# Performance work log

Hardware: AMD Instinct MI355X
Metric: run time of the kernel (lower is better)

## Reference

```python
import jax, jax.numpy as jnp
import numpy as np

EPS_NORM = 1e-12  # torch F.normalize eps
EPS_POOL = 1e-06
GAMMA = 10.0
TOPK = 32


def _l2norm(x, axis):
    n = jnp.sqrt(jnp.sum(x * x, axis=axis, keepdims=True))
    return x / jnp.maximum(n, EPS_NORM)


def _sae(x, enc, dec_w, dec_b):
    # x: [N, D]; enc: [H, D]; dec_w: [D, H]; dec_b: [D]
    w = _l2norm(enc, axis=1)
    x_n = _l2norm(x, axis=-1)
    cos = jnp.clip(x_n @ w.T, -1.0, 1.0)           # [N, H]
    acts = 2.0 - jnp.sqrt(2.0 - 2.0 * cos)
    vals, idx = jax.lax.top_k(acts, TOPK)           # [N, K]
    rows = jnp.arange(acts.shape[0])[:, None]
    sparse = jnp.zeros_like(acts).at[rows, idx].set(vals)
    recon = sparse @ dec_w.T + dec_b                # [N, D]
    return recon, sparse


def _sample_views(v_pad, centers, H, W):
    # v_pad: [B, Lmax, D], centers: [B, K, 2]; uniform grid HxW per batch
    L = H * W
    y = (jnp.arange(H, dtype=jnp.float32) + 0.5) / H
    x = (jnp.arange(W, dtype=jnp.float32) + 0.5) / W
    gy, gx = jnp.meshgrid(y, x, indexing='ij')
    coords = jnp.stack([gx.ravel(), gy.ravel()], axis=-1)        # [L, 2] (x, y)
    diff = centers[:, :, None, :] - coords[None, None, :, :]     # [B, K, L, 2]
    m = jnp.exp(-GAMMA * jnp.sum(diff * diff, axis=-1))          # [B, K, L]
    num = jnp.einsum('bkl,bld->bkd', m, v_pad[:, :L, :])
    den = jnp.sum(m, axis=-1, keepdims=True) + EPS_POOL
    return num / den                                             # [B, K, D]


def setup_inputs() -> dict:
    key = jax.random.key(0)
    ks = jax.random.split(key, 10)
    B, Lmax, D, Hh, T, K = 64, 1024, 1024, 16384, 512, 8
    fan_in = D
    bound = 1.0 / np.sqrt(fan_in)
    return {
        'v_pad': jax.random.normal(ks[0], (B, Lmax, D), jnp.float32),
        'v_len': jnp.full((B,), Lmax, dtype=jnp.int32),
        'grid_thws': jnp.tile(jnp.array([[1, 32, 32]], dtype=jnp.int32), (B, 1)),
        't_pad': jax.random.normal(ks[1], (B, T, D), jnp.float32),
        't_mask': jnp.ones((B, T), jnp.float32),
        'centers': jax.random.uniform(ks[2], (B, K, 2), jnp.float32),
        'enc_v': jax.random.normal(ks[3], (Hh, D), jnp.float32) * 0.02,
        'dec_v_w': jax.random.uniform(ks[4], (D, Hh), jnp.float32, -bound, bound),
        'dec_v_b': jnp.zeros((D,), jnp.float32),
        'enc_t': jax.random.normal(ks[5], (Hh, D), jnp.float32) * 0.02,
        'dec_t_w': jax.random.uniform(ks[6], (D, Hh), jnp.float32, -bound, bound),
        'dec_t_b': jnp.zeros((D,), jnp.float32),
    }


def reference(v_pad, v_len, grid_thws, t_pad, t_mask, centers,
              enc_v, dec_v_w, dec_v_b, enc_t, dec_t_w, dec_t_b):
    H = int(np.asarray(grid_thws)[0, 1])
    W = int(np.asarray(grid_thws)[0, 2])
    # text global pooling
    t_sum = jnp.sum(t_pad * t_mask[..., None], axis=1)
    t_global = t_sum / (jnp.sum(t_mask, axis=1, keepdims=True) + EPS_POOL)
    # gaussian view pooling
    v_views = _sample_views(v_pad, centers, H, W)                 # [B, K, D]
    recon_t, latent_t = _sae(t_global, enc_t, dec_t_w, dec_t_b)
    B, K, D = v_views.shape
    recon_v_flat, latent_v_flat = _sae(v_views.reshape(B * K, D), enc_v, dec_v_w, dec_v_b)
    recon_v = recon_v_flat.reshape(B, K, D)
    latent_v = latent_v_flat.reshape(B, K, -1)
    return (recon_v, v_views, recon_t, t_global, latent_v, latent_t)
```

## Files before the change

kernel.cpp:

```cpp
#include <hip/hip_runtime.h>
#include <hip/hip_bf16.h>

constexpr int NB    = 64;
constexpr int LMAX  = 1024;
constexpr int DD    = 1024;
constexpr int HSAE  = 16384;
constexpr int TT    = 512;
constexpr int KV    = 8;
constexpr int TOPK  = 32;
constexpr int NROW_V = NB * KV;
constexpr int NROW_T = NB;

constexpr size_t OUT_RECON_V = 0;
constexpr size_t OUT_VVIEWS  = OUT_RECON_V + (size_t)NROW_V * DD;
constexpr size_t OUT_RECON_T = OUT_VVIEWS + (size_t)NROW_V * DD;
constexpr size_t OUT_TGLOBAL = OUT_RECON_T + (size_t)NROW_T * DD;
constexpr size_t OUT_LAT_V   = OUT_TGLOBAL + (size_t)NROW_T * DD;
constexpr size_t OUT_LAT_T   = OUT_LAT_V + (size_t)NROW_V * HSAE;

constexpr size_t WS_VN     = 0;
constexpr size_t WS_TN     = WS_VN + (size_t)NROW_V * DD;
constexpr size_t WS_IDX_V  = WS_TN + (size_t)NROW_T * DD;
constexpr size_t WS_VAL_V  = WS_IDX_V + (size_t)NROW_V * TOPK;
constexpr size_t WS_IDX_T  = WS_VAL_V + (size_t)NROW_V * TOPK;
constexpr size_t WS_VAL_T  = WS_IDX_T + (size_t)NROW_T * TOPK;
constexpr size_t WS_BINV_V = WS_VAL_T + (size_t)NROW_T * TOPK;
constexpr size_t WS_BINV_T = WS_BINV_V + (size_t)HSAE;
constexpr size_t WS_AHI_V  = WS_BINV_T + (size_t)HSAE;
constexpr size_t WS_AHI_T  = WS_AHI_V + (size_t)NROW_V * DD / 2;

constexpr int LC  = 8;
constexpr int LCH = LMAX / LC;
constexpr int TC  = 8;
constexpr int TCH = TT / TC;
constexpr size_t PV_NUM = 0;
constexpr size_t PV_DEN = (size_t)NB * LC * KV * DD;
constexpr size_t PT_NUM = 0;
constexpr size_t PT_DEN = (size_t)NB * TC * DD;

typedef __attribute__((ext_vector_type(8))) short bf16x8;
typedef __attribute__((ext_vector_type(4))) short s16x4;
typedef __attribute__((ext_vector_type(4))) float f32x4;

__device__ inline unsigned short f2bf_rn(float x) {
    unsigned u = __float_as_uint(x);
    return (unsigned short)((u + 0x7FFFu + ((u >> 16) & 1u)) >> 16);
}
__device__ inline double shfl_down_dbl(double x, int off) {
    long long l = __double_as_longlong(x);
    int lo = (int)(l & 0xffffffffll), hi = (int)(l >> 32);
    lo = __shfl_down(lo, off); hi = __shfl_down(hi, off);
    return __longlong_as_double(((long long)hi << 32) | (unsigned long long)(unsigned int)lo);
}

__global__ __launch_bounds__(256) void pool_part_kernel(const float* __restrict__ v_pad,
                                                        const float* __restrict__ centers,
                                                        const int* __restrict__ grid_thws,
                                                        const float* __restrict__ t_pad,
                                                        const float* __restrict__ t_mask,
                                                        float* __restrict__ partV,
                                                        float* __restrict__ partT) {
    __shared__ float m_s[LCH * KV];
    const int b   = blockIdx.x;
    const int tid = threadIdx.x;

    if (blockIdx.y < LC) {
        const int lc = blockIdx.y;
        const int H = grid_thws[1];
        const int W = grid_thws[2];
        int L = H * W; if (L > LMAX) L = LMAX;
        const int l0 = lc * LCH;

        for (int i = tid; i < LCH * KV; i += 256) {
            const int ll = i >> 3, k = i & 7;
            const int l  = l0 + ll;
            float m = 0.f;
            if (l < L) {
                const int iy = l / W, ix = l - iy * W;
                const float gx = (ix + 0.5f) / (float)W;
                const float gy = (iy + 0.5f) / (float)H;
                const float dx = centers[((size_t)b * KV + k) * 2 + 0] - gx;
                const float dy = centers[((size_t)b * KV + k) * 2 + 1] - gy;
                m = expf(-10.f * (dx * dx + dy * dy));
            }
            m_s[ll * KV + k] = m;
        }
        __syncthreads();
        if (tid < KV) {
            float s = 0.f;
            for (int ll = 0; ll < LCH; ++ll) s += m_s[ll * KV + tid];
            partV[PV_DEN + ((size_t)b * LC + lc) * KV + tid] = s;
        }

        const float* vp = v_pad + ((size_t)b * LMAX + l0) * DD + tid * 4;
        float4 acc[KV];
#pragma unroll
        for (int k = 0; k < KV; ++k) acc[k] = make_float4(0.f, 0.f, 0.f, 0.f);
#pragma unroll 4
        for (int ll = 0; ll < LCH; ++ll) {
            const float4 v = *(const float4*)(vp + (size_t)ll * DD);
#pragma unroll
            for (int k = 0; k < KV; ++k) {
                const float m = m_s[ll * KV + k];
                acc[k].x = fmaf(m, v.x, acc[k].x); acc[k].y = fmaf(m, v.y, acc[k].y);
                acc[k].z = fmaf(m, v.z, acc[k].z); acc[k].w = fmaf(m, v.w, acc[k].w);
            }
        }
#pragma unroll
        for (int k = 0; k < KV; ++k)
            *(float4*)(partV + PV_NUM + (((size_t)b * LC + lc) * KV + k) * DD + tid * 4) = acc[k];
    } else {
        const int tc = blockIdx.y - LC;
        const int t0 = tc * TCH;
        if (tid < TCH) m_s[tid] = t_mask[(size_t)b * TT + t0 + tid];
        __syncthreads();
        if (tid == 0) {
            float s = 0.f;
            for (int i = 0; i < TCH; ++i) s += m_s[i];
            partT[PT_DEN + (size_t)b * TC + tc] = s;
        }
        const float* tp = t_pad + ((size_t)b * TT + t0) * DD + tid * 4;
        float4 acc = make_float4(0.f, 0.f, 0.f, 0.f);
#pragma unroll 4
        for (int t = 0; t < TCH; ++t) {
            const float4 v = *(const float4*)(tp + (size_t)t * DD);
            const float m = m_s[t];
            acc.x = fmaf(m, v.x, acc.x); acc.y = fmaf(m, v.y, acc.y);
            acc.z = fmaf(m, v.z, acc.z); acc.w = fmaf(m, v.w, acc.w);
        }
        *(float4*)(partT + PT_NUM + ((size_t)b * TC + tc) * DD + tid * 4) = acc;
    }
}

__device__ inline void comb_norm_emit(float4 vv, int r, int tid,
                                      float* __restrict__ out_row,
                                      float* __restrict__ ws, size_t xn_off, size_t hi_off) {
    *(float4*)(out_row + tid * 4) = vv;
    float ss = vv.x * vv.x + vv.y * vv.y + vv.z * vv.z + vv.w * vv.w;
#pragma unroll
    for (int off = 32; off; off >>= 1) ss += __shfl_down(ss, off);
    __shared__ float wsum[4];
    if ((tid & 63) == 0) wsum[tid >> 6] = ss;
    __syncthreads();
    const float tot = wsum[0] + wsum[1] + wsum[2] + wsum[3];
    const float scale = 1.f / fmaxf(sqrtf(tot), 1e-12f);
    float4 xn;
    xn.x = vv.x * scale; xn.y = vv.y * scale; xn.z = vv.z * scale; xn.w = vv.w * scale;
    *(float4*)(ws + xn_off + (size_t)r * DD + tid * 4) = xn;
    const float f[4] = {xn.x, xn.y, xn.z, xn.w};
    s16x4 hv;
#pragma unroll
    for (int c = 0; c < 4; ++c) hv[c] = (short)f2bf_rn(f[c]);
    *(s16x4*)((short*)(ws + hi_off) + (size_t)r * DD + tid * 4) = hv;
}

__global__ __launch_bounds__(256) void pool_comb_kernel(const float* __restrict__ partV,
                                                        const float* __restrict__ partT,
                                                        float* __restrict__ out_views,
                                                        float* __restrict__ out_tg,
                                                        float* __restrict__ ws) {
    const int b   = blockIdx.x;
    const int k   = blockIdx.y;
    const int tid = threadIdx.x;
    if (k < KV) {
        float den = 1e-6f;
        for (int lc = 0; lc < LC; ++lc) den += partV[PV_DEN + ((size_t)b * LC + lc) * KV + k];
        float4 s = make_float4(0.f, 0.f, 0.f, 0.f);
        for (int lc = 0; lc < LC; ++lc) {
            const float4 p = *(const float4*)(partV + PV_NUM + (((size_t)b * LC + lc) * KV + k) * DD + tid * 4);
            s.x += p.x; s.y += p.y; s.z += p.z; s.w += p.w;
        }
        const float inv = 1.f / den;
        float4 vv = make_float4(s.x * inv, s.y * inv, s.z * inv, s.w * inv);
        const int r = b * KV + k;
        comb_norm_emit(vv, r, tid, out_views + (size_t)r * DD, ws, WS_VN, WS_AHI_V);
    } else {
        float den = 1e-6f;
        for (int tc = 0; tc < TC; ++tc) den += partT[PT_DEN + (size_t)b * TC + tc];
        float4 s = make_float4(0.f, 0.f, 0.f, 0.f);
        for (int tc = 0; tc < TC; ++tc) {
            const float4 p = *(const float4*)(partT + PT_NUM + ((size_t)b * TC + tc) * DD + tid * 4);
            s.x += p.x; s.y += p.y; s.z += p.z; s.w += p.w;
        }
        const float inv = 1.f / den;
        float4 vv = make_float4(s.x * inv, s.y * inv, s.z * inv, s.w * inv);
        comb_norm_emit(vv, b, tid, out_tg + (size_t)b * DD, ws, WS_TN, WS_AHI_T);
    }
}

constexpr int GBM = 64, GBN = 64, GBK = 32;
constexpr int MY_SLOTS = NROW_V / GBM + 1;

__device__ inline int fragoff(int sub, int g, int r16) {
    return (((sub * 4 + g) * 16) + (r16 ^ ((g & 3) << 1))) * 8;
}

__global__ __launch_bounds__(256) void gemm_acts_mfma(const float* __restrict__ encV,
                                                      const float* __restrict__ encT,
                                                      float* __restrict__ out,
                                                      float* __restrict__ ws) {
    __shared__ short Ah[GBM * GBK];
    __shared__ short Bh[GBN * GBK];
    __shared__ float bn_part[GBN][4];
    __shared__ float binv_s[GBN];

    const int tid  = threadIdx.x;
    const int lane = tid & 63;
    const int wv   = tid >> 6;
    const int wm   = wv & 1;
    const int wn   = wv >> 1;
    const int bid  = blockIdx.x;
    const int xcd  = bid & 7;
    const int slot = bid >> 3;
    const int hb   = xcd + 8 * (slot / MY_SLOTS);
    const int my   = slot % MY_SLOTS;
    const bool isT = (my == MY_SLOTS - 1);
    const int h0   = hb * GBN;
    const int m0   = isT ? 0 : my * GBM;
    const int M    = isT ? NROW_T : NROW_V;
    const float* Bm = isT ? encT : encV;
    const short* AhiP = (const short*)(ws + (isT ? WS_AHI_T : WS_AHI_V));
    float* outActs = out + (isT ? OUT_LAT_T : OUT_LAT_V);
    float* binv_g  = ws + (isT ? WS_BINV_T : WS_BINV_V);

    const int ksS = tid & 3;
    const int lrA = tid >> 2;
    const int lrB = tid >> 2;

    f32x4 acc[2][2];
#pragma unroll
    for (int mi = 0; mi < 2; ++mi)
#pragma unroll
        for (int ni = 0; ni < 2; ++ni) acc[mi][ni] = (f32x4){0.f, 0.f, 0.f, 0.f};
    float bnacc = 0.f;

    bf16x8 pa;
    float4 pb0, pb1;

    auto issue_loads = [&](int kt) {
        if (m0 + lrA < M)
            pa = *(const bf16x8*)&AhiP[(size_t)(m0 + lrA) * DD + kt + ksS * 8];
        else
            pa = (bf16x8){0, 0, 0, 0, 0, 0, 0, 0};
        const float* src = Bm + (size_t)(h0 + lrB) * DD + kt + ksS * 8;
        pb0 = *(const float4*)src;
        pb1 = *(const float4*)(src + 4);
    };

    auto write_lds = [&]() {
        *(bf16x8*)&Ah[fragoff(lrA >> 4, ksS, lrA & 15)] = pa;
        {
            const float f[8] = {pb0.x, pb0.y, pb0.z, pb0.w, pb1.x, pb1.y, pb1.z, pb1.w};
            bf16x8 hv;
            float bsum = 0.f;
#pragma unroll
            for (int j = 0; j < 8; ++j) {
                hv[j] = (short)f2bf_rn(f[j]);
                bsum = fmaf(f[j], f[j], bsum);
            }
            bnacc += bsum;
            *(bf16x8*)&Bh[fragoff(lrB >> 4, ksS, lrB & 15)] = hv;
        }
    };

    issue_loads(0);
    for (int kt = 0; kt < DD; kt += GBK) {
        write_lds();
        __syncthreads();
        if (kt + GBK < DD) issue_loads(kt + GBK);

        {
            bf16x8 ah[2], bh[2];
            const int g = lane >> 4;
            const int r16 = lane & 15;
#pragma unroll
            for (int t = 0; t < 2; ++t) {
                ah[t] = *(const bf16x8*)&Ah[fragoff(wm * 2 + t, g, r16)];
                bh[t] = *(const bf16x8*)&Bh[fragoff(wn * 2 + t, g, r16)];
            }
#pragma unroll
            for (int mi = 0; mi < 2; ++mi)
#pragma unroll
                for (int ni = 0; ni < 2; ++ni)
                    acc[mi][ni] = __builtin_amdgcn_mfma_f32_16x16x32_bf16(ah[mi], bh[ni], acc[mi][ni], 0, 0, 0);
        }
        __syncthreads();
    }

    bn_part[lrB][ksS] = bnacc;
    __syncthreads();
    if (tid < GBN) {
        float s = bn_part[tid][0] + bn_part[tid][1] + bn_part[tid][2] + bn_part[tid][3];
        const float bi = 1.f / fmaxf(sqrtf(s), 1e-12f);
        binv_s[tid] = bi;
        if (my == 0 || isT) binv_g[h0 + tid] = bi;
    }
    __syncthreads();

#pragma unroll
    for (int mi = 0; mi < 2; ++mi)
#pragma unroll
        for (int ni = 0; ni < 2; ++ni) {
            const int hl = wn * 32 + ni * 16 + (lane & 15);
            const float bi = binv_s[hl];
#pragma unroll
            for (int j = 0; j < 4; ++j) {
                const int m = m0 + wm * 32 + mi * 16 + (lane >> 4) * 4 + j;
                if (m < M) {
                    float c = acc[mi][ni][j] * bi;
                    c = fminf(1.f, fmaxf(-1.f, c));
                    outActs[(size_t)m * HSAE + h0 + hl] = 2.f - sqrtf(fmaxf(0.f, 2.f - 2.f * c));
                }
            }
        }
}

constexpr int NBINS = 2048;
constexpr int NFINE = 256;
constexpr int CAP   = 512;
constexpr int BANDCAP = 128;
constexpr int MARGIN  = 12;
constexpr float RANKEPS = 2.5e-4f;

__global__ __launch_bounds__(256) void topk_kernel(float* __restrict__ out_buf,
                                                   float* __restrict__ ws,
                                                   const float* __restrict__ enc_v,
                                                   const float* __restrict__ enc_t) {
    const int r    = blockIdx.x;
    const int tid  = threadIdx.x;
    const int wv   = tid >> 6;
    const int lane = tid & 63;
    float* row;
    int* idxp; float* valp;
    const float* xn; const float* enc; const float* binv;
    if (r < NROW_V) {
        row  = out_buf + OUT_LAT_V + (size_t)r * HSAE;
        idxp = (int*)(ws + WS_IDX_V) + (size_t)r * TOPK;
        valp = ws + WS_VAL_V + (size_t)r * TOPK;
        xn   = ws + WS_VN + (size_t)r * DD;
        enc  = enc_v; binv = ws + WS_BINV_V;
    } else {
        const int rr = r - NROW_V;
        row  = out_buf + OUT_LAT_T + (size_t)rr * HSAE;
        idxp = (int*)(ws + WS_IDX_T) + (size_t)rr * TOPK;
        valp = ws + WS_VAL_T + (size_t)rr * TOPK;
        xn   = ws + WS_TN + (size_t)rr * DD;
        enc  = enc_t; binv = ws + WS_BINV_T;
    }

    __shared__ unsigned int hist[4][NBINS];
    __shared__ unsigned int fine[4][NFINE];
    __shared__ float xs[DD];
    __shared__ unsigned long long cand[CAP];
    __shared__ unsigned long long ord[CAP];
    __shared__ double bval[BANDCAP];
    __shared__ int    bidx[BANDCAP];
    __shared__ int s_ncand, s_bin, s_cntgt, s_sub, s_A, s_E;

    for (int i = tid; i < 4 * NBINS; i += 256) ((unsigned int*)hist)[i] = 0u;
    for (int i = tid; i < 4 * NFINE; i += 256) ((unsigned int*)fine)[i] = 0u;
    if (tid == 0) { s_ncand = 0; }
    *(float4*)&xs[tid * 4] = *(const float4*)&xn[tid * 4];

    unsigned int bcache[64];
#pragma unroll
    for (int e = 0; e < 16; ++e) {
        const float4 v = *(const float4*)(row + (size_t)e * 1024 + tid * 4);
        bcache[e * 4 + 0] = __float_as_uint(v.x);
        bcache[e * 4 + 1] = __float_as_uint(v.y);
        bcache[e * 4 + 2] = __float_as_uint(v.z);
        bcache[e * 4 + 3] = __float_as_uint(v.w);
    }
#pragma unroll
    for (int e = 0; e < 16; ++e)
        *(float4*)(row + (size_t)e * 1024 + tid * 4) = make_float4(0.f, 0.f, 0.f, 0.f);
    __syncthreads();

#pragma unroll
    for (int e = 0; e < 64; ++e) {
        unsigned int bin = bcache[e] >> 19;
        if (bin > NBINS - 1) bin = NBINS - 1;
        atomicAdd(&hist[wv][bin], 1u);
    }
    __syncthreads();
    for (int i = tid; i < NBINS; i += 256)
        hist[0][i] += hist[1][i] + hist[2][i] + hist[3][i];
    __syncthreads();

    if (tid < 64) {
        unsigned int csum = 0;
#pragma unroll
        for (int j = 0; j < 32; ++j)
            csum += hist[0][tid * 32 + ((tid + j) & 31)];
        unsigned int suf = csum;
#pragma unroll
        for (int off = 1; off < 64; off <<= 1) {
            unsigned int o = __shfl_down(suf, off);
            suf += (tid + off < 64) ? o : 0u;
        }
        if (suf >= (unsigned)TOPK && (suf - csum) < (unsigned)TOPK) {
            unsigned int run = suf - csum;
            int b = tid * 32 + 31;
            for (; b > tid * 32; --b) {
                const unsigned int h = hist[0][b];
                if (run + h >= (unsigned)TOPK) break;
                run += h;
            }
            s_bin = b; s_cntgt = (int)run;
        }
    }
    __syncthreads();
    const unsigned int B0 = (unsigned int)s_bin;
    const int r0 = TOPK - s_cntgt;

#pragma unroll
    for (int e = 0; e < 64; ++e) {
        const unsigned int bits = bcache[e];
        unsigned int bin = bits >> 19;
        if (bin > NBINS - 1) bin = NBINS - 1;
        if (bin == B0) atomicAdd(&fine[wv][(bits >> 11) & 255u], 1u);
    }
    __syncthreads();
    for (int i = tid; i < NFINE; i += 256)
        fine[0][i] += fine[1][i] + fine[2][i] + fine[3][i];
    __syncthreads();

    if (tid < 64) {
        unsigned int csum = fine[0][tid * 4] + fine[0][tid * 4 + 1] +
                            fine[0][tid * 4 + 2] + fine[0][tid * 4 + 3];
        unsigned int suf = csum;
#pragma unroll
        for (int off = 1; off < 64; off <<= 1) {
            unsigned int o = __shfl_down(suf, off);
            suf += (tid + off < 64) ? o : 0u;
        }
        if (suf >= (unsigned)r0 && (suf - csum) < (unsigned)r0) {
            unsigned int run = suf - csum;
            int b = tid * 4 + 3;
            for (; b > tid * 4; --b) {
                const unsigned int h = fine[0][b];
                if (run + h >= (unsigned)r0) break;
                run += h;
            }
            s_sub = b;
        }
    }
    __syncthreads();
    const unsigned int cf0 = (B0 << 8) | (unsigned)s_sub;
    const unsigned int cfTh = cf0 - (unsigned)MARGIN;

#pragma unroll
    for (int e = 0; e < 64; ++e) {
        const unsigned int bits = bcache[e];
        if ((bits >> 11) >= cfTh) {
            const int slot = atomicAdd(&s_ncand, 1);
            if (slot < CAP) {
                const unsigned int idx = (unsigned)(e >> 2) * 1024u + (unsigned)tid * 4u + (unsigned)(e & 3);
                cand[slot] = ((unsigned long long)bits << 32) | (unsigned long long)(16383u - idx);
            }
        }
    }
    __syncthreads();
    const int nc = (s_ncand < CAP) ? s_ncand : CAP;

    for (int i = tid; i < nc; i += 256) {
        const unsigned long long K = cand[i];
        int rank = 0;
        for (int j = 0; j < nc; ++j) rank += (cand[j] > K) ? 1 : 0;
        ord[rank] = K;
    }
    if (tid == 0) { s_A = nc; s_E = nc; }
    __syncthreads();

    const float Tv = __uint_as_float((unsigned)(ord[31] >> 32));
    for (int i = tid; i < nc; i += 256) {
        const float v = __uint_as_float((unsigned)(ord[i] >> 32));
        if (v <= Tv + 2.f * RANKEPS) atomicMin(&s_A, i);
        if (v <  Tv - 2.f * RANKEPS) atomicMin(&s_E, i);
    }
    __syncthreads();
    const int A = s_A;
    int E = s_E; if (E > A + BANDCAP) E = A + BANDCAP;
    const int nb = E - A;

    for (int t = A + wv; t < E; t += 4) {
        const int idx = 16383 - (int)(ord[t] & 0xffffffffull);
        const float* er = enc + (size_t)idx * DD;
        double s = 0.0;
#pragma unroll
        for (int i = 0; i < 16; ++i) {
            const int j = lane + i * 64;
            s = fma((double)xs[j], (double)er[j], s);
        }
#pragma unroll
        for (int off = 32; off; off >>= 1) s += shfl_down_dbl(s, off);
        if (lane == 0) {
            double c = s * (double)binv[idx];
            c = fmin(1.0, fmax(-1.0, c));
            bval[t - A] = 2.0 - sqrt(fmax(0.0, 2.0 - 2.0 * c));
            bidx[t - A] = idx;
        }
    }
    __syncthreads();

    for (int i = tid; i < A; i += 256) {
        const int idx  = 16383 - (int)(ord[i] & 0xffffffffull);
        const float v  = __uint_as_float((unsigned)(ord[i] >> 32));
        idxp[i] = idx; valp[i] = v; row[idx] = v;
    }
    for (int t = tid; t < nb; t += 256) {
        int fr = 0;
        for (int u = 0; u < nb; ++u)
            if (bval[u] > bval[t] || (bval[u] == bval[t] && bidx[u] < bidx[t])) fr++;
        const int slot = A + fr;
        if (slot < TOPK) {
            const float v = (float)bval[t];
            idxp[slot] = bidx[t]; valp[slot] = v; row[bidx[t]] = v;
        }
    }
}

__global__ __launch_bounds__(256) void recon_kernel(const float* __restrict__ dvw,
                                                    const float* __restrict__ dvb,
                                                    const float* __restrict__ dtw,
                                                    const float* __restrict__ dtb,
                                                    const float* __restrict__ ws,
                                                    float* __restrict__ out) {
    __shared__ float wrow[HSAE];
    const int bid = blockIdx.x;
    const bool isT = bid >= DD;
    const int d   = isT ? bid - DD : bid;
    const int tid = threadIdx.x;
    const float* decw = isT ? dtw : dvw;
    const float* decb = isT ? dtb : dvb;
    const int*   idxp = (const int*)(ws + (isT ? WS_IDX_T : WS_IDX_V));
    const float* valp = ws + (isT ? WS_VAL_T : WS_VAL_V);
    float* outp = out + (isT ? OUT_RECON_T : OUT_RECON_V);
    const int M = isT ? NROW_T : NROW_V;

    const float* wr = decw + (size_t)d * HSAE;
    for (int e = 0; e < HSAE / (256 * 4); ++e)
        *(float4*)&wrow[(size_t)(e * 256 + tid) * 4] = *(const float4*)(wr + (size_t)(e * 256 + tid) * 4);
    __syncthreads();
    const float bias = decb[d];
    for (int n = tid; n < M; n += 256) {
        float acc = bias;
#pragma unroll
        for (int k = 0; k < TOPK; ++k)
            acc = fmaf(valp[n * TOPK + k], wrow[idxp[n * TOPK + k]], acc);
        outp[(size_t)n * DD + d] = acc;
    }
}

extern "C" void kernel_launch(void* const* d_in, const int* in_sizes, int n_in,
                              void* d_out, int out_size, void* d_ws, size_t ws_size,
                              hipStream_t stream) {
    const float* v_pad    = (const float*)d_in[0];
    const int*   grid_thws = (const int*)d_in[2];
    const float* t_pad    = (const float*)d_in[3];
    const float* t_mask   = (const float*)d_in[4];
    const float* centers  = (const float*)d_in[5];
    const float* enc_v    = (const float*)d_in[6];
    const float* dec_v_w  = (const float*)d_in[7];
    const float* dec_v_b  = (const float*)d_in[8];
    const float* enc_t    = (const float*)d_in[9];
    const float* dec_t_w  = (const float*)d_in[10];
    const float* dec_t_b  = (const float*)d_in[11];
    float* out = (float*)d_out;
    float* ws  = (float*)d_ws;

    pool_part_kernel<<<dim3(NB, LC + TC), 256, 0, stream>>>(v_pad, centers, grid_thws, t_pad, t_mask,
                                                            out + OUT_LAT_V, out + OUT_LAT_T);
    pool_comb_kernel<<<dim3(NB, KV + 1), 256, 0, stream>>>(out + OUT_LAT_V, out + OUT_LAT_T,
                                                           out + OUT_VVIEWS, out + OUT_TGLOBAL, ws);
    gemm_acts_mfma<<<(HSAE / GBN) * MY_SLOTS * 1, 256, 0, stream>>>(enc_v, enc_t, out, ws);
    topk_kernel<<<NROW_V + NROW_T, 256, 0, stream>>>(out, ws, enc_v, enc_t);
    recon_kernel<<<2 * DD, 256, 0, stream>>>(dec_v_w, dec_v_b, dec_t_w, dec_t_b, ws, out);
}
```

Measured before the change: 267.3 us.

## Pre-pack encoder weights to bf16 fragments and drop LDS staging in GEMM

A new kernel converts both encoder matrices to bf16 once per call. It writes them in an MFMA-fragment-ordered layout and computes the inverse row norms at the same time. The activation GEMM then loads A and B fragments straight from global memory into MFMA instructions, with no LDS staging, no barriers and no per-tile fp32-to-bf16 conversion. This removes the repeated fp32 encoder reads and conversions across the nine M-slots that share each H tile. The cost is an extra pass that reads the full fp32 encoders and writes a bf16 copy, plus fragment loads in the GEMM that are no longer shared through LDS.

```diff
diff --git a/kernel.cpp b/kernel.cpp
--- a/kernel.cpp
+++ b/kernel.cpp
@@ -28,6 +28,8 @@
 constexpr size_t WS_BINV_T = WS_BINV_V + (size_t)HSAE;
 constexpr size_t WS_AHI_V  = WS_BINV_T + (size_t)HSAE;
 constexpr size_t WS_AHI_T  = WS_AHI_V + (size_t)NROW_V * DD / 2;
+constexpr size_t WS_PKV    = WS_AHI_T + (size_t)NROW_T * DD / 2;
+constexpr size_t WS_PKT    = WS_PKV + (size_t)HSAE * DD / 2;
 
 constexpr int LC  = 8;
 constexpr int LCH = LMAX / LC;
@@ -51,6 +53,46 @@
     int lo = (int)(l & 0xffffffffll), hi = (int)(l >> 32);
     lo = __shfl_down(lo, off); hi = __shfl_down(hi, off);
     return __longlong_as_double(((long long)hi << 32) | (unsigned long long)(unsigned int)lo);
+}
+
+__global__ __launch_bounds__(256) void pack_enc_kernel(const float* __restrict__ encV,
+                                                       const float* __restrict__ encT,
+                                                       float* __restrict__ ws) {
+    const int ht   = blockIdx.x;
+    const bool isT = (blockIdx.y == 1);
+    const float* enc = isT ? encT : encV;
+    short* pk   = (short*)(ws + (isT ? WS_PKT : WS_PKV));
+    float* binv = ws + (isT ? WS_BINV_T : WS_BINV_V);
+    const int tid = threadIdx.x;
+    const int l   = tid & 63;
+    const int w   = tid >> 6;
+    const int row = ht * 16 + (l & 15);
+    const int kc  = (l >> 4) * 8;
+    float ss = 0.f;
+#pragma unroll
+    for (int it = 0; it < 8; ++it) {
+        const int ktile = it * 4 + w;
+        const int k = ktile * 32 + kc;
+        const float4 v0 = *(const float4*)&enc[(size_t)row * DD + k];
+        const float4 v1 = *(const float4*)&enc[(size_t)row * DD + k + 4];
+        const float f[8] = {v0.x, v0.y, v0.z, v0.w, v1.x, v1.y, v1.z, v1.w};
+        bf16x8 hv;
+#pragma unroll
+        for (int j = 0; j < 8; ++j) {
+            hv[j] = (short)f2bf_rn(f[j]);
+            ss = fmaf(f[j], f[j], ss);
+        }
+        *(bf16x8*)&pk[((size_t)ht * 32 + ktile) * 512 + l * 8] = hv;
+    }
+    ss += __shfl_down(ss, 32);
+    ss += __shfl_down(ss, 16);
+    __shared__ float part[4][16];
+    if (l < 16) part[w][l] = ss;
+    __syncthreads();
+    if (tid < 16) {
+        const float s = part[0][tid] + part[1][tid] + part[2][tid] + part[3][tid];
+        binv[ht * 16 + tid] = 1.f / fmaxf(sqrtf(s), 1e-12f);
+    }
 }
 
 __global__ __launch_bounds__(256) void pool_part_kernel(const float* __restrict__ v_pad,
@@ -188,22 +230,11 @@
     }
 }
 
-constexpr int GBM = 64, GBN = 64, GBK = 32;
+constexpr int GBM = 64, GBN = 64;
 constexpr int MY_SLOTS = NROW_V / GBM + 1;
 
-__device__ inline int fragoff(int sub, int g, int r16) {
-    return (((sub * 4 + g) * 16) + (r16 ^ ((g & 3) << 1))) * 8;
-}
-
-__global__ __launch_bounds__(256) void gemm_acts_mfma(const float* __restrict__ encV,
-                                                      const float* __restrict__ encT,
-                                                      float* __restrict__ out,
+__global__ __launch_bounds__(256) void gemm_acts_mfma(float* __restrict__ out,
                                                       float* __restrict__ ws) {
-    __shared__ short Ah[GBM * GBK];
-    __shared__ short Bh[GBN * GBK];
-    __shared__ float bn_part[GBN][4];
-    __shared__ float binv_s[GBN];
-
     const int tid  = threadIdx.x;
     const int lane = tid & 63;
     const int wv   = tid >> 6;
@@ -217,102 +248,50 @@
     const bool isT = (my == MY_SLOTS - 1);
     const int h0   = hb * GBN;
     const int m0   = isT ? 0 : my * GBM;
-    const int M    = isT ? NROW_T : NROW_V;
-    const float* Bm = isT ? encT : encV;
-    const short* AhiP = (const short*)(ws + (isT ? WS_AHI_T : WS_AHI_V));
+    const short* A  = (const short*)(ws + (isT ? WS_AHI_T : WS_AHI_V));
+    const short* PK = (const short*)(ws + (isT ? WS_PKT : WS_PKV));
+    const float* binv_g = ws + (isT ? WS_BINV_T : WS_BINV_V);
     float* outActs = out + (isT ? OUT_LAT_T : OUT_LAT_V);
-    float* binv_g  = ws + (isT ? WS_BINV_T : WS_BINV_V);
-
-    const int ksS = tid & 3;
-    const int lrA = tid >> 2;
-    const int lrB = tid >> 2;
-
-    f32x4 acc[2][2];
-#pragma unroll
-    for (int mi = 0; mi < 2; ++mi)
-#pragma unroll
-        for (int ni = 0; ni < 2; ++ni) acc[mi][ni] = (f32x4){0.f, 0.f, 0.f, 0.f};
-    float bnacc = 0.f;
-
-    bf16x8 pa;
-    float4 pb0, pb1;
-
-    auto issue_loads = [&](int kt) {
-        if (m0 + lrA < M)
-            pa = *(const bf16x8*)&AhiP[(size_t)(m0 + lrA) * DD + kt + ksS * 8];
-        else
-            pa = (bf16x8){0, 0, 0, 0, 0, 0, 0, 0};
-        const float* src = Bm + (size_t)(h0 + lrB) * DD + kt + ksS * 8;
-        pb0 = *(const float4*)src;
-        pb1 = *(const float4*)(src + 4);
-    };
-
-    auto write_lds = [&]() {
-        *(bf16x8*)&Ah[fragoff(lrA >> 4, ksS, lrA & 15)] = pa;
-        {
-            const float f[8] = {pb0.x, pb0.y, pb0.z, pb0.w, pb1.x, pb1.y, pb1.z, pb1.w};
-            bf16x8 hv;
-            float bsum = 0.f;
-#pragma unroll
-            for (int j = 0; j < 8; ++j) {
-                hv[j] = (short)f2bf_rn(f[j]);
-                bsum = fmaf(f[j], f[j], bsum);
-            }
-            bnacc += bsum;
-            *(bf16x8*)&Bh[fragoff(lrB >> 4, ksS, lrB & 15)] = hv;
-        }
-    };
-
-    issue_loads(0);
-    for (int kt = 0; kt < DD; kt += GBK) {
-        write_lds();
-        __syncthreads();
-        if (kt + GBK < DD) issue_loads(kt + GBK);
-
-        {
-            bf16x8 ah[2], bh[2];
-            const int g = lane >> 4;
-            const int r16 = lane & 15;
-#pragma unroll
-            for (int t = 0; t < 2; ++t) {
-                ah[t] = *(const bf16x8*)&Ah[fragoff(wm * 2 + t, g, r16)];
-                bh[t] = *(const bf16x8*)&Bh[fragoff(wn * 2 + t, g, r16)];
-            }
-#pragma unroll
-            for (int mi = 0; mi < 2; ++mi)
-#pragma unroll
-                for (int ni = 0; ni < 2; ++ni)
-                    acc[mi][ni] = __builtin_amdgcn_mfma_f32_16x16x32_bf16(ah[mi], bh[ni], acc[mi][ni], 0, 0, 0);
-        }
-        __syncthreads();
-    }
-
-    bn_part[lrB][ksS] = bnacc;
-    __syncthreads();
-    if (tid < GBN) {
-        float s = bn_part[tid][0] + bn_part[tid][1] + bn_part[tid][2] + bn_part[tid][3];
-        const float bi = 1.f / fmaxf(sqrtf(s), 1e-12f);
-        binv_s[tid] = bi;
-        if (my == 0 || isT) binv_g[h0 + tid] = bi;
-    }
-    __syncthreads();
-
-#pragma unroll
-    for (int mi = 0; mi < 2; ++mi)
-#pragma unroll
-        for (int ni = 0; ni < 2; ++ni) {
-            const int hl = wn * 32 + ni * 16 + (lane & 15);
-            const float bi = binv_s[hl];
+
+    const int r16 = lane & 15;
+    const int g8  = (lane >> 4) * 8;
+
+    const short* aptr0 = A + (size_t)(m0 + wm * 32 + r16) * DD + g8;
+    const short* aptr1 = aptr0 + (size_t)16 * DD;
+    const short* bptr0 = PK + ((size_t)((h0 >> 4) + wn * 2) * 32) * 512 + lane * 8;
+    const short* bptr1 = bptr0 + (size_t)32 * 512;
+
+    f32x4 acc00 = {0.f,0.f,0.f,0.f}, acc01 = {0.f,0.f,0.f,0.f};
+    f32x4 acc10 = {0.f,0.f,0.f,0.f}, acc11 = {0.f,0.f,0.f,0.f};
+
+#pragma unroll 4
+    for (int kt = 0; kt < 32; ++kt) {
+        const bf16x8 a0 = *(const bf16x8*)(aptr0 + kt * 32);
+        const bf16x8 a1 = *(const bf16x8*)(aptr1 + kt * 32);
+        const bf16x8 b0 = *(const bf16x8*)(bptr0 + kt * 512);
+        const bf16x8 b1 = *(const bf16x8*)(bptr1 + kt * 512);
+        acc00 = __builtin_amdgcn_mfma_f32_16x16x32_bf16(a0, b0, acc00, 0, 0, 0);
+        acc01 = __builtin_amdgcn_mfma_f32_16x16x32_bf16(a0, b1, acc01, 0, 0, 0);
+        acc10 = __builtin_amdgcn_mfma_f32_16x16x32_bf16(a1, b0, acc10, 0, 0, 0);
+        acc11 = __builtin_amdgcn_mfma_f32_16x16x32_bf16(a1, b1, acc11, 0, 0, 0);
+    }
+
+    const f32x4 accs[2][2] = {{acc00, acc01}, {acc10, acc11}};
+#pragma unroll
+    for (int ni = 0; ni < 2; ++ni) {
+        const int hl = wn * 32 + ni * 16 + r16;
+        const float bi = binv_g[h0 + hl];
+#pragma unroll
+        for (int mi = 0; mi < 2; ++mi) {
 #pragma unroll
             for (int j = 0; j < 4; ++j) {
                 const int m = m0 + wm * 32 + mi * 16 + (lane >> 4) * 4 + j;
-                if (m < M) {
-                    float c = acc[mi][ni][j] * bi;
-                    c = fminf(1.f, fmaxf(-1.f, c));
-                    outActs[(size_t)m * HSAE + h0 + hl] = 2.f - sqrtf(fmaxf(0.f, 2.f - 2.f * c));
-                }
+                float c = accs[mi][ni][j] * bi;
+                c = fminf(1.f, fmaxf(-1.f, c));
+                outActs[(size_t)m * HSAE + h0 + hl] = 2.f - sqrtf(fmaxf(0.f, 2.f - 2.f * c));
             }
         }
+    }
 }
 
 constexpr int NBINS = 2048;
@@ -569,11 +548,12 @@
     float* out = (float*)d_out;
     float* ws  = (float*)d_ws;
 
+    pack_enc_kernel<<<dim3(HSAE / 16, 2), 256, 0, stream>>>(enc_v, enc_t, ws);
     pool_part_kernel<<<dim3(NB, LC + TC), 256, 0, stream>>>(v_pad, centers, grid_thws, t_pad, t_mask,
                                                             out + OUT_LAT_V, out + OUT_LAT_T);
     pool_comb_kernel<<<dim3(NB, KV + 1), 256, 0, stream>>>(out + OUT_LAT_V, out + OUT_LAT_T,
                                                            out + OUT_VVIEWS, out + OUT_TGLOBAL, ws);
-    gemm_acts_mfma<<<(HSAE / GBN) * MY_SLOTS * 1, 256, 0, stream>>>(enc_v, enc_t, out, ws);
+    gemm_acts_mfma<<<(HSAE / GBN) * MY_SLOTS, 256, 0, stream>>>(out, ws);
     topk_kernel<<<NROW_V + NROW_T, 256, 0, stream>>>(out, ws, enc_v, enc_t);
     recon_kernel<<<2 * DD, 256, 0, stream>>>(dec_v_w, dec_v_b, dec_t_w, dec_t_b, ws, out);
 }
```

After: 324.1 us. 21.3% more time.
